# Optimization experiments

Hardware: AMD Instinct MI355X
Metric: run time of the kernel (lower is better)

The kernel has to match this reference:

```python
import jax, jax.numpy as jnp
import numpy as np

NUM_EMBEDDINGS = 1024
EMBEDDING_DIM = 64
COMMITMENT_COST = 0.25


def setup_inputs() -> dict:
    key = jax.random.key(0)
    kz, kc = jax.random.split(key)
    z = jax.random.normal(kz, (16, 2048, EMBEDDING_DIM), dtype=jnp.float32)
    # nn.Embedding weight init: uniform(-1/K, 1/K)
    codebook = (jax.random.uniform(kc, (NUM_EMBEDDINGS, EMBEDDING_DIM), dtype=jnp.float32) * 2.0 - 1.0) / NUM_EMBEDDINGS
    return {"z": z, "codebook": codebook}


def reference(z, codebook):
    D = codebook.shape[1]
    K = codebook.shape[0]
    flat_z = z.reshape(-1, D)  # [N, D]
    # squared L2 distances: ||z||^2 + ||e||^2 - 2 z.e  -> [N, K]
    distances = (
        jnp.sum(flat_z ** 2, axis=1, keepdims=True)
        + jnp.sum(codebook ** 2, axis=1)
        - 2.0 * jnp.matmul(flat_z, codebook.T)
    )
    encoding_indices = jnp.argmin(distances, axis=1)  # [N]
    quantized = codebook[encoding_indices].reshape(z.shape)

    e_latent_loss = jnp.mean((jax.lax.stop_gradient(quantized) - z) ** 2)
    q_latent_loss = jnp.mean((quantized - jax.lax.stop_gradient(z)) ** 2)
    vq_loss = q_latent_loss + COMMITMENT_COST * e_latent_loss

    # straight-through estimator
    quantized_st = z + jax.lax.stop_gradient(quantized - z)

    # perplexity from codebook usage histogram
    n = encoding_indices.shape[0]
    counts = jnp.zeros((K,), dtype=jnp.float32).at[encoding_indices].add(1.0)
    avg_probs = counts / n
    perplexity = jnp.exp(-jnp.sum(avg_probs * jnp.log(avg_probs + 1e-10)))

    indices_out = encoding_indices.reshape(z.shape[:-1])
    return quantized_st, vq_loss, indices_out, perplexity
```

## Files before the change

kernel.cpp:

```cpp
#include <hip/hip_runtime.h>
#include <math.h>


#define D 64
#define KC 1024
#define MT 4
#define ROWS (MT * 16)

typedef short short8 __attribute__((ext_vector_type(8)));
typedef short short4v __attribute__((ext_vector_type(4)));
typedef float f32x4 __attribute__((ext_vector_type(4)));

__device__ __forceinline__ unsigned short f2bf(float x) {
  unsigned int u = __float_as_uint(x);
  unsigned int r = (u + 0x7fffu + ((u >> 16) & 1u)) >> 16;
  return (unsigned short)r;
}
__device__ __forceinline__ float bf2f(unsigned short h) {
  return __uint_as_float((unsigned int)h << 16);
}

__global__ __launch_bounds__(256) void vq_prep(
    const float* __restrict__ cb, unsigned short* __restrict__ bsplit,
    float* __restrict__ cbn, unsigned int* __restrict__ hist,
    float* __restrict__ loss_acc) {
  const int k = blockIdx.x * 256 + threadIdx.x;
  const float4* e = (const float4*)(cb + (size_t)k * D);
  unsigned short* bp = bsplit + (size_t)k * 128;
  float s0 = 0.f, s1 = 0.f, s2 = 0.f, s3 = 0.f;
#pragma unroll
  for (int i = 0; i < 16; ++i) {
    float4 v = e[i];
    s0 = fmaf(v.x, v.x, s0);
    s1 = fmaf(v.y, v.y, s1);
    s2 = fmaf(v.z, v.z, s2);
    s3 = fmaf(v.w, v.w, s3);
    unsigned short h0 = f2bf(v.x), h1 = f2bf(v.y), h2 = f2bf(v.z), h3 = f2bf(v.w);
    short4v hv = {(short)h0, (short)h1, (short)h2, (short)h3};
    short4v lv = {(short)f2bf(v.x - bf2f(h0)), (short)f2bf(v.y - bf2f(h1)),
                  (short)f2bf(v.z - bf2f(h2)), (short)f2bf(v.w - bf2f(h3))};
    *(short4v*)(bp + i * 4) = hv;
    *(short4v*)(bp + 64 + i * 4) = lv;
  }
  cbn[k] = (s0 + s1) + (s2 + s3);
  hist[k] = 0u;
  if (k == 0) loss_acc[0] = 0.f;
}

__global__ __launch_bounds__(256, 2) void vq_main(
    const float* __restrict__ z, const unsigned short* __restrict__ bsplit,
    const float* __restrict__ cbn, const float* __restrict__ cb,
    float* __restrict__ out_q, float* __restrict__ out_idx,
    unsigned int* __restrict__ hist, float* __restrict__ loss_acc) {
  __shared__ unsigned short Ash[ROWS * 136];
  __shared__ float srzp[ROWS * 16];
  __shared__ float srz[ROWS];
  __shared__ float candd[4][ROWS][17];
  __shared__ int candk[4][ROWS][17];
  __shared__ int skf[ROWS];
  __shared__ float swav[4];
  __shared__ unsigned int lhist[KC];

  const int tid = threadIdx.x;
  const int lane = tid & 63;
  const int wav = tid >> 6;
  const int quad = lane >> 4;
  const int col = lane & 15;
  const int rowbase = blockIdx.x * ROWS;

  const float4* z4 = (const float4*)(z + (size_t)rowbase * D);
#pragma unroll
  for (int it = 0; it < ROWS / 16; ++it) {
    int f4 = it * 256 + tid;
    int row = f4 >> 4, c4 = (f4 & 15) * 4;
    float4 v = z4[f4];
    srzp[f4] = ((v.x * v.x + v.y * v.y) + (v.z * v.z + v.w * v.w));
    unsigned short h0 = f2bf(v.x), h1 = f2bf(v.y), h2 = f2bf(v.z), h3 = f2bf(v.w);
    short4v hv = {(short)h0, (short)h1, (short)h2, (short)h3};
    short4v lv = {(short)f2bf(v.x - bf2f(h0)), (short)f2bf(v.y - bf2f(h1)),
                  (short)f2bf(v.z - bf2f(h2)), (short)f2bf(v.w - bf2f(h3))};
    *(short4v*)&Ash[row * 136 + c4] = hv;
    *(short4v*)&Ash[row * 136 + 64 + c4] = lv;
  }
#pragma unroll
  for (int j = 0; j < KC / 256; ++j) lhist[tid + 256 * j] = 0u;
  __syncthreads();
  if (tid < ROWS) {
    float s = 0.f;
#pragma unroll
    for (int i = 0; i < 16; ++i) s += srzp[tid * 16 + i];
    srz[tid] = s;
  }
  __syncthreads();

  float rzv[MT * 4];
#pragma unroll
  for (int mt = 0; mt < MT; ++mt)
#pragma unroll
    for (int reg = 0; reg < 4; ++reg)
      rzv[mt * 4 + reg] = srz[mt * 16 + quad * 4 + reg];

  short8 a[MT][4];
#pragma unroll
  for (int mt = 0; mt < MT; ++mt) {
    const unsigned short* base = &Ash[(mt * 16 + col) * 136 + quad * 8];
    a[mt][0] = *(const short8*)(base + 0);
    a[mt][1] = *(const short8*)(base + 32);
    a[mt][2] = *(const short8*)(base + 64);
    a[mt][3] = *(const short8*)(base + 96);
  }

  float bestd[MT * 4];
  int bestk[MT * 4];
#pragma unroll
  for (int i = 0; i < MT * 4; ++i) {
    bestd[i] = 3.4e38f;
    bestk[i] = 0;
  }

  const int k0 = wav * 256;
  short8 p0[4], p1[4];
  float pe0, pe1;
  {
    const unsigned short* b0p = bsplit + (size_t)(k0 + col) * 128 + quad * 8;
    p0[0] = *(const short8*)(b0p + 0);
    p0[1] = *(const short8*)(b0p + 32);
    p0[2] = *(const short8*)(b0p + 64);
    p0[3] = *(const short8*)(b0p + 96);
    pe0 = cbn[k0 + col];
    const unsigned short* b1p = bsplit + (size_t)(k0 + 16 + col) * 128 + quad * 8;
    p1[0] = *(const short8*)(b1p + 0);
    p1[1] = *(const short8*)(b1p + 32);
    p1[2] = *(const short8*)(b1p + 64);
    p1[3] = *(const short8*)(b1p + 96);
    pe1 = cbn[k0 + 16 + col];
  }

  for (int it = 0; it < 8; ++it) {
    const short8 c00 = p0[0], c01 = p0[1], c02 = p0[2], c03 = p0[3];
    const short8 c10 = p1[0], c11 = p1[1], c12 = p1[2], c13 = p1[3];
    const float ce0 = pe0, ce1 = pe1;
    const int kbase = k0 + it * 32;
    if (it < 7) {
      const unsigned short* n0 =
          bsplit + (size_t)(kbase + 32 + col) * 128 + quad * 8;
      p0[0] = *(const short8*)(n0 + 0);
      p0[1] = *(const short8*)(n0 + 32);
      p0[2] = *(const short8*)(n0 + 64);
      p0[3] = *(const short8*)(n0 + 96);
      pe0 = cbn[kbase + 32 + col];
      const unsigned short* n1 =
          bsplit + (size_t)(kbase + 48 + col) * 128 + quad * 8;
      p1[0] = *(const short8*)(n1 + 0);
      p1[1] = *(const short8*)(n1 + 32);
      p1[2] = *(const short8*)(n1 + 64);
      p1[3] = *(const short8*)(n1 + 96);
      pe1 = cbn[kbase + 48 + col];
    }

    {
      f32x4 acc[MT];
#pragma unroll
      for (int mt = 0; mt < MT; ++mt) acc[mt] = {0.f, 0.f, 0.f, 0.f};
#pragma unroll
      for (int mt = 0; mt < MT; ++mt)
        acc[mt] = __builtin_amdgcn_mfma_f32_16x16x32_bf16(a[mt][0], c00, acc[mt], 0, 0, 0);
#pragma unroll
      for (int mt = 0; mt < MT; ++mt)
        acc[mt] = __builtin_amdgcn_mfma_f32_16x16x32_bf16(a[mt][1], c01, acc[mt], 0, 0, 0);
#pragma unroll
      for (int mt = 0; mt < MT; ++mt)
        acc[mt] = __builtin_amdgcn_mfma_f32_16x16x32_bf16(a[mt][2], c00, acc[mt], 0, 0, 0);
#pragma unroll
      for (int mt = 0; mt < MT; ++mt)
        acc[mt] = __builtin_amdgcn_mfma_f32_16x16x32_bf16(a[mt][3], c01, acc[mt], 0, 0, 0);
#pragma unroll
      for (int mt = 0; mt < MT; ++mt)
        acc[mt] = __builtin_amdgcn_mfma_f32_16x16x32_bf16(a[mt][0], c02, acc[mt], 0, 0, 0);
#pragma unroll
      for (int mt = 0; mt < MT; ++mt)
        acc[mt] = __builtin_amdgcn_mfma_f32_16x16x32_bf16(a[mt][1], c03, acc[mt], 0, 0, 0);
      const int mycode = kbase + col;
#pragma unroll
      for (int mt = 0; mt < MT; ++mt)
#pragma unroll
        for (int reg = 0; reg < 4; ++reg) {
          float dist = fmaf(-2.0f, acc[mt][reg], rzv[mt * 4 + reg] + ce0);
          int i = mt * 4 + reg;
          bool better = dist < bestd[i];
          bestk[i] = better ? mycode : bestk[i];
          bestd[i] = better ? dist : bestd[i];
        }
    }
    {
      f32x4 acc[MT];
#pragma unroll
      for (int mt = 0; mt < MT; ++mt) acc[mt] = {0.f, 0.f, 0.f, 0.f};
#pragma unroll
      for (int mt = 0; mt < MT; ++mt)
        acc[mt] = __builtin_amdgcn_mfma_f32_16x16x32_bf16(a[mt][0], c10, acc[mt], 0, 0, 0);
#pragma unroll
      for (int mt = 0; mt < MT; ++mt)
        acc[mt] = __builtin_amdgcn_mfma_f32_16x16x32_bf16(a[mt][1], c11, acc[mt], 0, 0, 0);
#pragma unroll
      for (int mt = 0; mt < MT; ++mt)
        acc[mt] = __builtin_amdgcn_mfma_f32_16x16x32_bf16(a[mt][2], c10, acc[mt], 0, 0, 0);
#pragma unroll
      for (int mt = 0; mt < MT; ++mt)
        acc[mt] = __builtin_amdgcn_mfma_f32_16x16x32_bf16(a[mt][3], c11, acc[mt], 0, 0, 0);
#pragma unroll
      for (int mt = 0; mt < MT; ++mt)
        acc[mt] = __builtin_amdgcn_mfma_f32_16x16x32_bf16(a[mt][0], c12, acc[mt], 0, 0, 0);
#pragma unroll
      for (int mt = 0; mt < MT; ++mt)
        acc[mt] = __builtin_amdgcn_mfma_f32_16x16x32_bf16(a[mt][1], c13, acc[mt], 0, 0, 0);
      const int mycode = kbase + 16 + col;
#pragma unroll
      for (int mt = 0; mt < MT; ++mt)
#pragma unroll
        for (int reg = 0; reg < 4; ++reg) {
          float dist = fmaf(-2.0f, acc[mt][reg], rzv[mt * 4 + reg] + ce1);
          int i = mt * 4 + reg;
          bool better = dist < bestd[i];
          bestk[i] = better ? mycode : bestk[i];
          bestd[i] = better ? dist : bestd[i];
        }
    }
  }

#pragma unroll
  for (int mt = 0; mt < MT; ++mt)
#pragma unroll
    for (int reg = 0; reg < 4; ++reg) {
      int row = mt * 16 + quad * 4 + reg;
      candd[wav][row][col] = bestd[mt * 4 + reg];
      candk[wav][row][col] = bestk[mt * 4 + reg];
    }
  __syncthreads();

  if (lane < 16) {
    const int row = wav * 16 + lane;
    float bd1 = 3.4e38f, bd2 = 3.4e38f;
    int bk1 = 0x7fffffff, bk2 = 0x7fffffff;
#pragma unroll
    for (int w = 0; w < 4; ++w)
      for (int c = 0; c < 16; ++c) {
        float dv = candd[w][row][c];
        int kv = candk[w][row][c];
        bool b1 = (dv < bd1) || (dv == bd1 && kv < bk1);
        bool b2 = (dv < bd2) || (dv == bd2 && kv < bk2);
        if (b1) {
          bd2 = bd1; bk2 = bk1;
          bd1 = dv; bk1 = kv;
        } else if (b2) {
          bd2 = dv; bk2 = kv;
        }
      }
    if (bd2 - bd1 < 1e-5f) {
      const int grow = rowbase + row;
      const float4* zp = (const float4*)(z + (size_t)grow * D);
      float s0 = 0.f, s1 = 0.f, s2 = 0.f, s3 = 0.f;
#pragma unroll
      for (int i = 0; i < 16; ++i) {
        float4 v = zp[i];
        s0 = fmaf(v.x, v.x, s0);
        s1 = fmaf(v.y, v.y, s1);
        s2 = fmaf(v.z, v.z, s2);
        s3 = fmaf(v.w, v.w, s3);
      }
      const float rzx = (s0 + s1) + (s2 + s3);
      float dx[2];
      int kk[2] = {bk1, bk2};
#pragma unroll
      for (int c = 0; c < 2; ++c) {
        const float4* e4 = (const float4*)(cb + (size_t)kk[c] * D);
        float d0 = 0.f, d1 = 0.f, d2 = 0.f, d3 = 0.f;
#pragma unroll
        for (int i = 0; i < 16; ++i) {
          float4 v = e4[i];
          float4 zv = zp[i];
          d0 = fmaf(zv.x, v.x, d0);
          d1 = fmaf(zv.y, v.y, d1);
          d2 = fmaf(zv.z, v.z, d2);
          d3 = fmaf(zv.w, v.w, d3);
        }
        float dot = (d0 + d1) + (d2 + d3);
        dx[c] = (rzx + cbn[kk[c]]) - 2.0f * dot;
      }
      if ((dx[1] < dx[0]) || (dx[1] == dx[0] && bk2 < bk1)) bk1 = bk2;
    }
    skf[row] = bk1;
    out_idx[rowbase + row] = (float)bk1;
    atomicAdd(&lhist[bk1], 1u);
  }
  __syncthreads();

#pragma unroll
  for (int j = 0; j < KC / 256; ++j) {
    unsigned int c = lhist[tid + 256 * j];
    if (c) atomicAdd(&hist[tid + 256 * j], c);
  }

  float lsum = 0.f;
#pragma unroll
  for (int it = 0; it < ROWS / 16; ++it) {
    int f4 = it * 256 + tid;
    int r = f4 >> 4;
    int c4 = (f4 & 15) * 4;
    int bk = skf[r];
    const float4 q = *(const float4*)(cb + (size_t)bk * D + c4);
    const int grow = rowbase + r;
    const float4 zv = *(const float4*)(z + (size_t)grow * D + c4);
    *(float4*)(out_q + (size_t)grow * D + c4) = q;
    float ax = q.x - zv.x, ay = q.y - zv.y, az = q.z - zv.z, aw = q.w - zv.w;
    lsum += ax * ax + ay * ay + az * az + aw * aw;
  }
#pragma unroll
  for (int off = 32; off > 0; off >>= 1) lsum += __shfl_down(lsum, off, 64);
  if (lane == 0) swav[wav] = lsum;
  __syncthreads();
  if (tid == 0) {
    atomicAdd(loss_acc, (swav[0] + swav[1]) + (swav[2] + swav[3]));
  }
}

__global__ __launch_bounds__(1024) void vq_final(
    const unsigned int* __restrict__ hist, const float* __restrict__ loss_acc,
    float* __restrict__ out_loss, float* __restrict__ out_perp, float inv_n,
    float inv_nd) {
  __shared__ float part[16];
  const int t = threadIdx.x;
  const int lane = t & 63;
  const int wav = t >> 6;
  float p = (float)hist[t] * inv_n;
  float v = p * logf(p + 1e-10f);
#pragma unroll
  for (int off = 32; off > 0; off >>= 1) v += __shfl_down(v, off, 64);
  if (lane == 0) part[wav] = v;
  __syncthreads();
  if (t == 0) {
    float s = 0.f;
#pragma unroll
    for (int j = 0; j < 16; ++j) s += part[j];
    *out_perp = expf(-s);
    *out_loss = 1.25f * loss_acc[0] * inv_nd;
  }
}

extern "C" void kernel_launch(void* const* d_in, const int* in_sizes, int n_in,
                              void* d_out, int out_size, void* d_ws,
                              size_t ws_size, hipStream_t stream) {
  (void)n_in;
  (void)out_size;
  (void)ws_size;
  const float* z = (const float*)d_in[0];
  const float* cb = (const float*)d_in[1];
  const int N = in_sizes[0] / D;

  float* out_q = (float*)d_out;
  float* out_loss = (float*)d_out + (size_t)N * D;
  float* out_idx = out_loss + 1;
  float* out_perp = out_idx + N;

  unsigned int* hist = (unsigned int*)d_ws;
  float* loss_acc = (float*)d_ws + 1024;
  float* cbn = (float*)d_ws + 1040;
  unsigned short* bsplit = (unsigned short*)((float*)d_ws + 2064);

  vq_prep<<<dim3(KC / 256), dim3(256), 0, stream>>>(cb, bsplit, cbn, hist,
                                                    loss_acc);
  vq_main<<<dim3(N / ROWS), dim3(256), 0, stream>>>(z, bsplit, cbn, cb, out_q,
                                                    out_idx, hist, loss_acc);
  vq_final<<<dim3(1), dim3(1024), 0, stream>>>(
      hist, loss_acc, out_loss, out_perp, 1.0f / (float)N,
      1.0f / ((float)N * (float)D));
}
```

Baseline: 102.7 us.

## Split VQ main kernel into separate score and writer kernels with z pre-split

Moves the bf16 hi/lo splitting of z and its row norms into the prep kernel, writing them to workspace. The main kernel becomes two kernels: a scoring kernel that reads pre-split z from global memory and writes the top-2 candidates per row, and a writer kernel that does the tie-break refinement, histogram, quantized output and loss. This shrinks shared-memory use and per-kernel register pressure in the MFMA scoring loop. The cost is extra global round trips for zsplit and the candidates, plus an additional kernel launch.

```diff
diff --git a/kernel.cpp b/kernel.cpp
--- a/kernel.cpp
+++ b/kernel.cpp
@@ -21,45 +21,70 @@
 }
 
 __global__ __launch_bounds__(256) void vq_prep(
-    const float* __restrict__ cb, unsigned short* __restrict__ bsplit,
-    float* __restrict__ cbn, unsigned int* __restrict__ hist,
-    float* __restrict__ loss_acc) {
-  const int k = blockIdx.x * 256 + threadIdx.x;
-  const float4* e = (const float4*)(cb + (size_t)k * D);
-  unsigned short* bp = bsplit + (size_t)k * 128;
-  float s0 = 0.f, s1 = 0.f, s2 = 0.f, s3 = 0.f;
-#pragma unroll
-  for (int i = 0; i < 16; ++i) {
-    float4 v = e[i];
-    s0 = fmaf(v.x, v.x, s0);
-    s1 = fmaf(v.y, v.y, s1);
-    s2 = fmaf(v.z, v.z, s2);
-    s3 = fmaf(v.w, v.w, s3);
-    unsigned short h0 = f2bf(v.x), h1 = f2bf(v.y), h2 = f2bf(v.z), h3 = f2bf(v.w);
-    short4v hv = {(short)h0, (short)h1, (short)h2, (short)h3};
-    short4v lv = {(short)f2bf(v.x - bf2f(h0)), (short)f2bf(v.y - bf2f(h1)),
-                  (short)f2bf(v.z - bf2f(h2)), (short)f2bf(v.w - bf2f(h3))};
-    *(short4v*)(bp + i * 4) = hv;
-    *(short4v*)(bp + 64 + i * 4) = lv;
-  }
-  cbn[k] = (s0 + s1) + (s2 + s3);
-  hist[k] = 0u;
-  if (k == 0) loss_acc[0] = 0.f;
-}
-
-__global__ __launch_bounds__(256, 2) void vq_main(
-    const float* __restrict__ z, const unsigned short* __restrict__ bsplit,
-    const float* __restrict__ cbn, const float* __restrict__ cb,
-    float* __restrict__ out_q, float* __restrict__ out_idx,
+    const float* __restrict__ cb, const float* __restrict__ z,
+    unsigned short* __restrict__ bsplit, unsigned short* __restrict__ zsplit,
+    float* __restrict__ cbn, float* __restrict__ rzn,
     unsigned int* __restrict__ hist, float* __restrict__ loss_acc) {
-  __shared__ unsigned short Ash[ROWS * 136];
-  __shared__ float srzp[ROWS * 16];
-  __shared__ float srz[ROWS];
+  __shared__ float srzp[1024];
+  const int b = blockIdx.x;
+  const int tid = threadIdx.x;
+  if (b < 4) {
+    const int k = b * 256 + tid;
+    const float4* e = (const float4*)(cb + (size_t)k * D);
+    unsigned short* bp = bsplit + (size_t)k * 128;
+    float s0 = 0.f, s1 = 0.f, s2 = 0.f, s3 = 0.f;
+#pragma unroll
+    for (int i = 0; i < 16; ++i) {
+      float4 v = e[i];
+      s0 = fmaf(v.x, v.x, s0);
+      s1 = fmaf(v.y, v.y, s1);
+      s2 = fmaf(v.z, v.z, s2);
+      s3 = fmaf(v.w, v.w, s3);
+      unsigned short h0 = f2bf(v.x), h1 = f2bf(v.y), h2 = f2bf(v.z),
+                     h3 = f2bf(v.w);
+      short4v hv = {(short)h0, (short)h1, (short)h2, (short)h3};
+      short4v lv = {(short)f2bf(v.x - bf2f(h0)), (short)f2bf(v.y - bf2f(h1)),
+                    (short)f2bf(v.z - bf2f(h2)), (short)f2bf(v.w - bf2f(h3))};
+      *(short4v*)(bp + i * 4) = hv;
+      *(short4v*)(bp + 64 + i * 4) = lv;
+    }
+    cbn[k] = (s0 + s1) + (s2 + s3);
+    hist[k] = 0u;
+    if (k == 0) loss_acc[0] = 0.f;
+  } else {
+    const int rowbase = (b - 4) * 64;
+    const float4* z4 = (const float4*)(z + (size_t)rowbase * D);
+#pragma unroll
+    for (int it = 0; it < 4; ++it) {
+      int f4 = it * 256 + tid;
+      int row = f4 >> 4, c4 = (f4 & 15) * 4;
+      float4 v = z4[f4];
+      srzp[f4] = ((v.x * v.x + v.y * v.y) + (v.z * v.z + v.w * v.w));
+      unsigned short h0 = f2bf(v.x), h1 = f2bf(v.y), h2 = f2bf(v.z),
+                     h3 = f2bf(v.w);
+      short4v hv = {(short)h0, (short)h1, (short)h2, (short)h3};
+      short4v lv = {(short)f2bf(v.x - bf2f(h0)), (short)f2bf(v.y - bf2f(h1)),
+                    (short)f2bf(v.z - bf2f(h2)), (short)f2bf(v.w - bf2f(h3))};
+      unsigned short* zp = zsplit + (size_t)(rowbase + row) * 128;
+      *(short4v*)(zp + c4) = hv;
+      *(short4v*)(zp + 64 + c4) = lv;
+    }
+    __syncthreads();
+    if (tid < 64) {
+      float s = 0.f;
+#pragma unroll
+      for (int i = 0; i < 16; ++i) s += srzp[tid * 16 + i];
+      rzn[rowbase + tid] = s;
+    }
+  }
+}
+
+__global__ __launch_bounds__(256, 2) void vq_score(
+    const unsigned short* __restrict__ zsplit, const float* __restrict__ rzn,
+    const unsigned short* __restrict__ bsplit, const float* __restrict__ cbn,
+    float* __restrict__ t2d, int* __restrict__ t2k) {
   __shared__ float candd[4][ROWS][17];
   __shared__ int candk[4][ROWS][17];
-  __shared__ int skf[ROWS];
-  __shared__ float swav[4];
-  __shared__ unsigned int lhist[KC];
 
   const int tid = threadIdx.x;
   const int lane = tid & 63;
@@ -68,47 +93,22 @@
   const int col = lane & 15;
   const int rowbase = blockIdx.x * ROWS;
 
-  const float4* z4 = (const float4*)(z + (size_t)rowbase * D);
-#pragma unroll
-  for (int it = 0; it < ROWS / 16; ++it) {
-    int f4 = it * 256 + tid;
-    int row = f4 >> 4, c4 = (f4 & 15) * 4;
-    float4 v = z4[f4];
-    srzp[f4] = ((v.x * v.x + v.y * v.y) + (v.z * v.z + v.w * v.w));
-    unsigned short h0 = f2bf(v.x), h1 = f2bf(v.y), h2 = f2bf(v.z), h3 = f2bf(v.w);
-    short4v hv = {(short)h0, (short)h1, (short)h2, (short)h3};
-    short4v lv = {(short)f2bf(v.x - bf2f(h0)), (short)f2bf(v.y - bf2f(h1)),
-                  (short)f2bf(v.z - bf2f(h2)), (short)f2bf(v.w - bf2f(h3))};
-    *(short4v*)&Ash[row * 136 + c4] = hv;
-    *(short4v*)&Ash[row * 136 + 64 + c4] = lv;
-  }
-#pragma unroll
-  for (int j = 0; j < KC / 256; ++j) lhist[tid + 256 * j] = 0u;
-  __syncthreads();
-  if (tid < ROWS) {
-    float s = 0.f;
-#pragma unroll
-    for (int i = 0; i < 16; ++i) s += srzp[tid * 16 + i];
-    srz[tid] = s;
-  }
-  __syncthreads();
-
-  float rzv[MT * 4];
-#pragma unroll
-  for (int mt = 0; mt < MT; ++mt)
-#pragma unroll
-    for (int reg = 0; reg < 4; ++reg)
-      rzv[mt * 4 + reg] = srz[mt * 16 + quad * 4 + reg];
-
   short8 a[MT][4];
 #pragma unroll
   for (int mt = 0; mt < MT; ++mt) {
-    const unsigned short* base = &Ash[(mt * 16 + col) * 136 + quad * 8];
+    const unsigned short* base =
+        zsplit + (size_t)(rowbase + mt * 16 + col) * 128 + quad * 8;
     a[mt][0] = *(const short8*)(base + 0);
     a[mt][1] = *(const short8*)(base + 32);
     a[mt][2] = *(const short8*)(base + 64);
     a[mt][3] = *(const short8*)(base + 96);
   }
+  float rzv[MT * 4];
+#pragma unroll
+  for (int mt = 0; mt < MT; ++mt)
+#pragma unroll
+    for (int reg = 0; reg < 4; ++reg)
+      rzv[mt * 4 + reg] = rzn[rowbase + mt * 16 + quad * 4 + reg];
 
   float bestd[MT * 4];
   int bestk[MT * 4];
@@ -128,7 +128,8 @@
     p0[2] = *(const short8*)(b0p + 64);
     p0[3] = *(const short8*)(b0p + 96);
     pe0 = cbn[k0 + col];
-    const unsigned short* b1p = bsplit + (size_t)(k0 + 16 + col) * 128 + quad * 8;
+    const unsigned short* b1p =
+        bsplit + (size_t)(k0 + 16 + col) * 128 + quad * 8;
     p1[0] = *(const short8*)(b1p + 0);
     p1[1] = *(const short8*)(b1p + 32);
     p1[2] = *(const short8*)(b1p + 64);
@@ -157,7 +158,6 @@
       p1[3] = *(const short8*)(n1 + 96);
       pe1 = cbn[kbase + 48 + col];
     }
-
     {
       f32x4 acc[MT];
 #pragma unroll
@@ -238,27 +238,55 @@
     }
   __syncthreads();
 
-  if (lane < 16) {
-    const int row = wav * 16 + lane;
+  if (tid < ROWS) {
     float bd1 = 3.4e38f, bd2 = 3.4e38f;
     int bk1 = 0x7fffffff, bk2 = 0x7fffffff;
 #pragma unroll
     for (int w = 0; w < 4; ++w)
       for (int c = 0; c < 16; ++c) {
-        float dv = candd[w][row][c];
-        int kv = candk[w][row][c];
-        bool b1 = (dv < bd1) || (dv == bd1 && kv < bk1);
-        bool b2 = (dv < bd2) || (dv == bd2 && kv < bk2);
-        if (b1) {
+        float dv = candd[w][tid][c];
+        int kv = candk[w][tid][c];
+        bool h1 = (dv < bd1) || (dv == bd1 && kv < bk1);
+        bool h2 = (dv < bd2) || (dv == bd2 && kv < bk2);
+        if (h1) {
           bd2 = bd1; bk2 = bk1;
           bd1 = dv; bk1 = kv;
-        } else if (b2) {
+        } else if (h2) {
           bd2 = dv; bk2 = kv;
         }
       }
+    const int row = rowbase + tid;
+    t2d[2 * row] = bd1;
+    t2d[2 * row + 1] = bd2;
+    t2k[2 * row] = bk1;
+    t2k[2 * row + 1] = bk2;
+  }
+}
+
+__global__ __launch_bounds__(256) void vq_writer(
+    const float* __restrict__ z, const float* __restrict__ cb,
+    const float* __restrict__ cbn, const float* __restrict__ t2d,
+    const int* __restrict__ t2k, float* __restrict__ out_q,
+    float* __restrict__ out_idx, unsigned int* __restrict__ hist,
+    float* __restrict__ loss_acc) {
+  __shared__ int skf[ROWS];
+  __shared__ unsigned int lhist[KC];
+  __shared__ float swav[4];
+  const int tid = threadIdx.x;
+  const int lane = tid & 63;
+  const int wav = tid >> 6;
+  const int rowbase = blockIdx.x * ROWS;
+
+#pragma unroll
+  for (int j = 0; j < KC / 256; ++j) lhist[tid + 256 * j] = 0u;
+  __syncthreads();
+
+  if (tid < ROWS) {
+    const int row = rowbase + tid;
+    float bd1 = t2d[2 * row], bd2 = t2d[2 * row + 1];
+    int bk1 = t2k[2 * row], bk2 = t2k[2 * row + 1];
     if (bd2 - bd1 < 1e-5f) {
-      const int grow = rowbase + row;
-      const float4* zp = (const float4*)(z + (size_t)grow * D);
+      const float4* zp = (const float4*)(z + (size_t)row * D);
       float s0 = 0.f, s1 = 0.f, s2 = 0.f, s3 = 0.f;
 #pragma unroll
       for (int i = 0; i < 16; ++i) {
@@ -289,8 +317,8 @@
       }
       if ((dx[1] < dx[0]) || (dx[1] == dx[0] && bk2 < bk1)) bk1 = bk2;
     }
-    skf[row] = bk1;
-    out_idx[rowbase + row] = (float)bk1;
+    skf[tid] = bk1;
+    out_idx[row] = (float)bk1;
     atomicAdd(&lhist[bk1], 1u);
   }
   __syncthreads();
@@ -303,7 +331,7 @@
 
   float lsum = 0.f;
 #pragma unroll
-  for (int it = 0; it < ROWS / 16; ++it) {
+  for (int it = 0; it < 4; ++it) {
     int f4 = it * 256 + tid;
     int r = f4 >> 4;
     int c4 = (f4 & 15) * 4;
@@ -319,9 +347,8 @@
   for (int off = 32; off > 0; off >>= 1) lsum += __shfl_down(lsum, off, 64);
   if (lane == 0) swav[wav] = lsum;
   __syncthreads();
-  if (tid == 0) {
+  if (tid == 0)
     atomicAdd(loss_acc, (swav[0] + swav[1]) + (swav[2] + swav[3]));
-  }
 }
 
 __global__ __launch_bounds__(1024) void vq_final(
@@ -366,11 +393,17 @@
   float* loss_acc = (float*)d_ws + 1024;
   float* cbn = (float*)d_ws + 1040;
   unsigned short* bsplit = (unsigned short*)((float*)d_ws + 2064);
-
-  vq_prep<<<dim3(KC / 256), dim3(256), 0, stream>>>(cb, bsplit, cbn, hist,
-                                                    loss_acc);
-  vq_main<<<dim3(N / ROWS), dim3(256), 0, stream>>>(z, bsplit, cbn, cb, out_q,
-                                                    out_idx, hist, loss_acc);
+  unsigned short* zsplit = (unsigned short*)((float*)d_ws + 67600);
+  float* rzn = (float*)d_ws + 2164752;
+  float* t2d = (float*)d_ws + 2197520;
+  int* t2k = (int*)((float*)d_ws + 2263056);
+
+  vq_prep<<<dim3(4 + N / 64), dim3(256), 0, stream>>>(cb, z, bsplit, zsplit,
+                                                      cbn, rzn, hist, loss_acc);
+  vq_score<<<dim3(N / ROWS), dim3(256), 0, stream>>>(zsplit, rzn, bsplit, cbn,
+                                                     t2d, t2k);
+  vq_writer<<<dim3(N / ROWS), dim3(256), 0, stream>>>(
+      z, cb, cbn, t2d, t2k, out_q, out_idx, hist, loss_acc);
   vq_final<<<dim3(1), dim3(1024), 0, stream>>>(
       hist, loss_acc, out_loss, out_perp, 1.0f / (float)N,
       1.0f / ((float)N * (float)D));
```

After: 114.6 us. +11.6%, slower.
